# Optimization experiments

Hardware: AMD Instinct MI355X
Metric: run time of the kernel (lower is better)

## Reference

```python
import jax, jax.numpy as jnp
import numpy as np

HEADS = 8
EPS = 1e-5


def setup_inputs() -> dict:
    key = jax.random.key(0)
    B, N, C = 32, 4096, 256
    headc = C // HEADS
    x = jax.random.normal(key, (B, N, C), dtype=jnp.float32)
    return {
        "x": x,
        "kln_weight": jnp.ones((HEADS, 1, headc), dtype=jnp.float32),
        "kln_bias": jnp.zeros((HEADS, 1, headc), dtype=jnp.float32),
        "vln_weight": jnp.ones((HEADS, 1, headc), dtype=jnp.float32),
        "vln_bias": jnp.zeros((HEADS, 1, headc), dtype=jnp.float32),
    }


def _ln(t, w, b, headc):
    # Faithful to the torch module: unbiased std (ddof=1), eps added to std (not var).
    m = jnp.mean(t, axis=-1, keepdims=True)
    d = t - m
    std = jnp.sqrt(jnp.sum(d * d, axis=-1, keepdims=True) / (headc - 1))
    return w * (d / (std + EPS)) + b


def reference(x, kln_weight, kln_bias, vln_weight, vln_bias):
    B, N, C = x.shape
    headc = C // HEADS
    # [B, H, N, D]
    qkv = x.reshape(B, N, HEADS, headc).transpose(0, 2, 1, 3)
    k = _ln(qkv, kln_weight, kln_bias, headc)
    v = _ln(qkv, vln_weight, vln_bias, headc)
    # k^T v : [B, H, D, D], scaled by 1/N
    kv = jnp.einsum("bhnd,bhne->bhde", k, v) / N
    # q (k^T v): [B, H, N, D]
    out = jnp.einsum("bhnd,bhde->bhne", qkv, kv)
    out = out.transpose(0, 2, 1, 3).reshape(B, N, C)
    return out + x
```

## Files before the change

kernel.cpp:

```cpp
#include <hip/hip_runtime.h>

#define H_ 8
#define D_ 32
#define B_ 32
#define N_ 4096
#define C_ 256
#define EPS_ 1e-5f

#define SLOT_ 1088

typedef __attribute__((ext_vector_type(8))) short bf16x8;
typedef __attribute__((ext_vector_type(4))) float f32x4;

__device__ __forceinline__ short f2bf(float f) {
    unsigned u = __builtin_bit_cast(unsigned, f);
    unsigned r = (u + 0x7FFFu + ((u >> 16) & 1u)) >> 16;
    return (short)r;
}

__device__ __forceinline__ int uidx(int r, int c) {
    return r * 40 + ((r >> 3) & 3) * 16 + c;
}

__global__ __launch_bounds__(256, 4)
void k1_skv(const float* __restrict__ x, float* __restrict__ Pws)
{
    __shared__ short ubuf[256 * 40 + 64];

    const int tid  = threadIdx.x;
    const int bh   = blockIdx.x >> 2;
    const int q4   = blockIdx.x & 3;
    const int b    = bh >> 3;
    const int h    = bh & 7;
    const int lane = tid & 63;
    const int wave = tid >> 6;
    const int g    = lane >> 4;
    const int cL   = lane & 15;

    f32x4 acc[2][2] = {};
    f32x4 tq[2] = {};

    bf16x8 ones;
    #pragma unroll
    for (int j = 0; j < 8; ++j) ones[j] = (short)0x3F80;

    const float* xbase = x + ((size_t)b * N_ + q4 * 1024 + tid) * C_ + h * D_;

    float4 xA[8], xB[8];
    #pragma unroll
    for (int c = 0; c < 8; ++c)
        xA[c] = reinterpret_cast<const float4*>(xbase)[c];

    auto body = [&](const float4 (&xr)[8], float4 (&nx)[8], int it, bool pf) {
        if (pf) {
            const float* p = xbase + (size_t)(it + 1) * 256 * C_;
            #pragma unroll
            for (int c = 0; c < 8; ++c)
                nx[c] = reinterpret_cast<const float4*>(p)[c];
        }

        float sum = 0.f, sq = 0.f;
        #pragma unroll
        for (int c = 0; c < 8; ++c) {
            const float4 a = xr[c];
            sum += a.x + a.y + a.z + a.w;
            sq = fmaf(a.x, a.x, fmaf(a.y, a.y, fmaf(a.z, a.z, fmaf(a.w, a.w, sq))));
        }
        const float m   = sum * (1.f / 32.f);
        const float ss  = fmaxf(sq - sum * m, 0.f);
        const float inv = 1.f / (sqrtf(ss * (1.f / 31.f)) + EPS_);

        {
            const int base = tid * 40 + ((tid >> 3) & 3) * 16;
            #pragma unroll
            for (int q = 0; q < 4; ++q) {
                const float4 a0 = xr[q * 2 + 0];
                const float4 a1 = xr[q * 2 + 1];
                bf16x8 wv;
                wv[0] = f2bf((a0.x - m) * inv); wv[1] = f2bf((a0.y - m) * inv);
                wv[2] = f2bf((a0.z - m) * inv); wv[3] = f2bf((a0.w - m) * inv);
                wv[4] = f2bf((a1.x - m) * inv); wv[5] = f2bf((a1.y - m) * inv);
                wv[6] = f2bf((a1.z - m) * inv); wv[7] = f2bf((a1.w - m) * inv);
                *reinterpret_cast<bf16x8*>(&ubuf[base + q * 8]) = wv;
            }
        }
        asm volatile("s_waitcnt lgkmcnt(0)" ::: "memory");

        #pragma unroll
        for (int ks = 0; ks < 2; ++ks) {
            const int R0 = wave * 64 + ks * 32 + 8 * g;
            bf16x8 F0, F1;
            #pragma unroll
            for (int j = 0; j < 8; ++j) {
                const int base = uidx(R0 + j, cL);
                F0[j] = ubuf[base];
                F1[j] = ubuf[base + 16];
            }
            tq[0] = __builtin_amdgcn_mfma_f32_16x16x32_bf16(ones, F0, tq[0], 0, 0, 0);
            tq[1] = __builtin_amdgcn_mfma_f32_16x16x32_bf16(ones, F1, tq[1], 0, 0, 0);
            acc[0][0] = __builtin_amdgcn_mfma_f32_16x16x32_bf16(F0, F0, acc[0][0], 0, 0, 0);
            acc[0][1] = __builtin_amdgcn_mfma_f32_16x16x32_bf16(F0, F1, acc[0][1], 0, 0, 0);
            acc[1][0] = __builtin_amdgcn_mfma_f32_16x16x32_bf16(F1, F0, acc[1][0], 0, 0, 0);
            acc[1][1] = __builtin_amdgcn_mfma_f32_16x16x32_bf16(F1, F1, acc[1][1], 0, 0, 0);
        }
    };

    body(xA, xB, 0, true);
    body(xB, xA, 1, true);
    body(xA, xB, 2, true);
    body(xB, xA, 3, false);

    __syncthreads();
    float* sred = reinterpret_cast<float*>(ubuf);
    {
        float* dst = sred + wave * 1024;
        #pragma unroll
        for (int ca = 0; ca < 2; ++ca)
            #pragma unroll
            for (int cb = 0; cb < 2; ++cb)
                #pragma unroll
                for (int r = 0; r < 4; ++r)
                    dst[(ca * 16 + g * 4 + r) * D_ + cb * 16 + cL] = acc[ca][cb][r];
    }
    if (lane < 16) {
        sred[4096 + wave * 32 + cL]      = tq[0][0];
        sred[4096 + wave * 32 + 16 + cL] = tq[1][0];
    }
    __syncthreads();

    float* slot = Pws + (size_t)blockIdx.x * SLOT_;
    {
        const float4 c0 = *reinterpret_cast<const float4*>(&sred[tid * 4]);
        const float4 c1 = *reinterpret_cast<const float4*>(&sred[1024 + tid * 4]);
        const float4 c2 = *reinterpret_cast<const float4*>(&sred[2048 + tid * 4]);
        const float4 c3 = *reinterpret_cast<const float4*>(&sred[3072 + tid * 4]);
        float4 o;
        o.x = c0.x + c1.x + c2.x + c3.x;
        o.y = c0.y + c1.y + c2.y + c3.y;
        o.z = c0.z + c1.z + c2.z + c3.z;
        o.w = c0.w + c1.w + c2.w + c3.w;
        *reinterpret_cast<float4*>(slot + tid * 4) = o;
    }
    if (tid < D_)
        slot[1024 + tid] = sred[4096 + tid] + sred[4096 + 32 + tid]
                         + sred[4096 + 64 + tid] + sred[4096 + 96 + tid];
}

__global__ __launch_bounds__(256, 4)
void k2_out(const float* __restrict__ x, const float* __restrict__ Pws,
            const float* __restrict__ kw, const float* __restrict__ kb,
            const float* __restrict__ vw, const float* __restrict__ vb,
            float* __restrict__ out)
{
    __shared__ float xbuf[4 * C_];

    const int tid   = threadIdx.x;
    const int b     = blockIdx.x >> 6;
    const int chunk = blockIdx.x & 63;
    const int h     = tid >> 5;
    const int e     = tid & 31;
    const int bh    = b * 8 + h;

    const float* P0 = Pws + (size_t)(bh * 4 + 0) * SLOT_;
    const float* P1 = Pws + (size_t)(bh * 4 + 1) * SLOT_;
    const float* P2 = Pws + (size_t)(bh * 4 + 2) * SLOT_;
    const float* P3 = Pws + (size_t)(bh * 4 + 3) * SLOT_;

    const float wve  = vw[h * D_ + e];
    const float bve  = vb[h * D_ + e];
    const float Te   = P0[1024 + e] + P1[1024 + e] + P2[1024 + e] + P3[1024 + e];
    const float invN = 1.f / (float)N_;

    float kvc[32];
    #pragma unroll
    for (int d = 0; d < D_; ++d) {
        const float Sde = P0[d * D_ + e] + P1[d * D_ + e]
                        + P2[d * D_ + e] + P3[d * D_ + e];
        const float Td  = P0[1024 + d] + P1[1024 + d] + P2[1024 + d] + P3[1024 + d];
        const float wkd = kw[h * D_ + d];
        const float bkd = kb[h * D_ + d];
        kvc[d] = invN * (wkd * (wve * Sde + bve * Td) + bkd * wve * Te)
               + bkd * bve;
    }

    for (int it = 0; it < 16; ++it) {
        const int r0 = chunk * 64 + it * 4;
        const float* xrow = x + ((size_t)b * N_ + r0) * C_;
        const float4 xv = reinterpret_cast<const float4*>(xrow)[tid];
        __syncthreads();
        reinterpret_cast<float4*>(xbuf)[tid] = xv;
        __syncthreads();

        float res[4];
        #pragma unroll
        for (int r = 0; r < 4; ++r) {
            const float4* xr4 = reinterpret_cast<const float4*>(xbuf + r * C_ + h * D_);
            float dot = 0.f;
            #pragma unroll
            for (int c = 0; c < 8; ++c) {
                const float4 a = xr4[c];
                dot += a.x * kvc[c * 4 + 0] + a.y * kvc[c * 4 + 1]
                     + a.z * kvc[c * 4 + 2] + a.w * kvc[c * 4 + 3];
            }
            res[r] = dot + xbuf[r * C_ + tid];
        }
        float* orow = out + ((size_t)b * N_ + r0) * C_;
        #pragma unroll
        for (int r = 0; r < 4; ++r) orow[r * C_ + tid] = res[r];
    }
}

extern "C" void kernel_launch(void* const* d_in, const int* in_sizes, int n_in,
                              void* d_out, int out_size, void* d_ws, size_t ws_size,
                              hipStream_t stream)
{
    const float* x  = (const float*)d_in[0];
    const float* kw = (const float*)d_in[1];
    const float* kb = (const float*)d_in[2];
    const float* vw = (const float*)d_in[3];
    const float* vb = (const float*)d_in[4];
    float* outp = (float*)d_out;

    float* Pws = (float*)d_ws;

    k1_skv<<<dim3(B_ * H_ * 4), dim3(256), 0, stream>>>(x, Pws);
    k2_out<<<dim3(B_ * 64), dim3(256), 0, stream>>>(x, Pws, kw, kb, vw, vb, outp);
}
```

Before: 101.3 us.

## Split kv reduction into separate kernel and pipeline output pass per wave

Moves the per-(b,h) reduction of partial S/T sums and the LN-affine fold into a new small kernel that writes a finished 32x32 kv matrix, so the output kernel no longer redoes that reduction in every block. The output kernel now has each wave handle two heads of a 64-column slice, double-buffers x rows in per-wave LDS with register prefetch, and drops the block-wide __syncthreads. This adds a third kernel launch and an extra round trip through the kv buffer in exchange for less redundant work and fewer barriers in the bandwidth-bound output pass.

```diff
diff --git a/kernel.cpp b/kernel.cpp
--- a/kernel.cpp
+++ b/kernel.cpp
@@ -147,66 +147,104 @@
 }
 
 __global__ __launch_bounds__(256, 4)
-void k2_out(const float* __restrict__ x, const float* __restrict__ Pws,
-            const float* __restrict__ kw, const float* __restrict__ kb,
-            const float* __restrict__ vw, const float* __restrict__ vb,
-            float* __restrict__ out)
-{
-    __shared__ float xbuf[4 * C_];
-
-    const int tid   = threadIdx.x;
-    const int b     = blockIdx.x >> 6;
-    const int chunk = blockIdx.x & 63;
-    const int h     = tid >> 5;
-    const int e     = tid & 31;
-    const int bh    = b * 8 + h;
+void k_red(const float* __restrict__ Pws,
+           const float* __restrict__ kw, const float* __restrict__ kb,
+           const float* __restrict__ vw, const float* __restrict__ vb,
+           float* __restrict__ kvF)
+{
+    const int bh  = blockIdx.x;
+    const int h   = bh & 7;
+    const int tid = threadIdx.x;
+    const int d   = tid >> 3;
+    const int e0  = (tid & 7) * 4;
 
     const float* P0 = Pws + (size_t)(bh * 4 + 0) * SLOT_;
     const float* P1 = Pws + (size_t)(bh * 4 + 1) * SLOT_;
     const float* P2 = Pws + (size_t)(bh * 4 + 2) * SLOT_;
     const float* P3 = Pws + (size_t)(bh * 4 + 3) * SLOT_;
-
-    const float wve  = vw[h * D_ + e];
-    const float bve  = vb[h * D_ + e];
-    const float Te   = P0[1024 + e] + P1[1024 + e] + P2[1024 + e] + P3[1024 + e];
     const float invN = 1.f / (float)N_;
 
+    const float4 s0 = *reinterpret_cast<const float4*>(P0 + d * D_ + e0);
+    const float4 s1 = *reinterpret_cast<const float4*>(P1 + d * D_ + e0);
+    const float4 s2 = *reinterpret_cast<const float4*>(P2 + d * D_ + e0);
+    const float4 s3 = *reinterpret_cast<const float4*>(P3 + d * D_ + e0);
+    float Sde[4] = { s0.x + s1.x + s2.x + s3.x, s0.y + s1.y + s2.y + s3.y,
+                     s0.z + s1.z + s2.z + s3.z, s0.w + s1.w + s2.w + s3.w };
+
+    const float Td  = P0[1024 + d] + P1[1024 + d] + P2[1024 + d] + P3[1024 + d];
+    const float wkd = kw[h * D_ + d];
+    const float bkd = kb[h * D_ + d];
+
+    float4 o;
+    float* op = &o.x;
+    #pragma unroll
+    for (int j = 0; j < 4; ++j) {
+        const int e = e0 + j;
+        const float Te  = P0[1024 + e] + P1[1024 + e] + P2[1024 + e] + P3[1024 + e];
+        const float wve = vw[h * D_ + e];
+        const float bve = vb[h * D_ + e];
+        op[j] = invN * (wkd * (wve * Sde[j] + bve * Td) + bkd * wve * Te)
+              + bkd * bve;
+    }
+    *reinterpret_cast<float4*>(kvF + (size_t)bh * 1024 + tid * 4) = o;
+}
+
+__global__ __launch_bounds__(256, 4)
+void k2_out(const float* __restrict__ x, const float* __restrict__ kvF,
+            float* __restrict__ out)
+{
+    __shared__ float lds[4][2][256];
+
+    const int tid  = threadIdx.x;
+    const int lane = tid & 63;
+    const int w    = tid >> 6;
+    const int hloc = lane >> 5;
+    const int e    = lane & 31;
+    const int R0   = blockIdx.x * 64;
+    const int b    = R0 >> 12;
+    const int n0   = R0 & (N_ - 1);
+    const int h    = 2 * w + hloc;
+
+    const float* kvp = kvF + ((size_t)(b * H_ + h)) * 1024 + e;
     float kvc[32];
     #pragma unroll
-    for (int d = 0; d < D_; ++d) {
-        const float Sde = P0[d * D_ + e] + P1[d * D_ + e]
-                        + P2[d * D_ + e] + P3[d * D_ + e];
-        const float Td  = P0[1024 + d] + P1[1024 + d] + P2[1024 + d] + P3[1024 + d];
-        const float wkd = kw[h * D_ + d];
-        const float bkd = kb[h * D_ + d];
-        kvc[d] = invN * (wkd * (wve * Sde + bve * Td) + bkd * wve * Te)
-               + bkd * bve;
-    }
-
-    for (int it = 0; it < 16; ++it) {
-        const int r0 = chunk * 64 + it * 4;
-        const float* xrow = x + ((size_t)b * N_ + r0) * C_;
-        const float4 xv = reinterpret_cast<const float4*>(xrow)[tid];
-        __syncthreads();
-        reinterpret_cast<float4*>(xbuf)[tid] = xv;
-        __syncthreads();
-
-        float res[4];
+    for (int d = 0; d < D_; ++d) kvc[d] = kvp[d * D_];
+
+    const int lrow = lane >> 4;
+    const int lcol = (lane & 15) * 4;
+    const float* xg = x + ((size_t)b * N_ + n0 + lrow) * C_ + w * 64 + lcol;
+    float* og = out + ((size_t)b * N_ + n0) * C_ + w * 64 + hloc * 32 + e;
+
+    float* buf0 = &lds[w][0][0];
+    float* buf1 = &lds[w][1][0];
+    const int wslot = lrow * 64 + lcol;
+
+    float4 pA = *reinterpret_cast<const float4*>(xg);
+    float4 pB = *reinterpret_cast<const float4*>(xg + (size_t)4 * C_);
+
+    #pragma unroll 4
+    for (int t = 0; t < 16; ++t) {
+        float* buf = (t & 1) ? buf1 : buf0;
+        *reinterpret_cast<float4*>(buf + wslot) = pA;
+        pA = pB;
+        if (t + 2 < 16)
+            pB = *reinterpret_cast<const float4*>(xg + (size_t)(t + 2) * 4 * C_);
+        asm volatile("s_waitcnt lgkmcnt(0)" ::: "memory");
+
         #pragma unroll
         for (int r = 0; r < 4; ++r) {
-            const float4* xr4 = reinterpret_cast<const float4*>(xbuf + r * C_ + h * D_);
+            const float4* row4 =
+                reinterpret_cast<const float4*>(buf + r * 64 + hloc * 32);
             float dot = 0.f;
             #pragma unroll
             for (int c = 0; c < 8; ++c) {
-                const float4 a = xr4[c];
+                const float4 a = row4[c];
                 dot += a.x * kvc[c * 4 + 0] + a.y * kvc[c * 4 + 1]
                      + a.z * kvc[c * 4 + 2] + a.w * kvc[c * 4 + 3];
             }
-            res[r] = dot + xbuf[r * C_ + tid];
-        }
-        float* orow = out + ((size_t)b * N_ + r0) * C_;
-        #pragma unroll
-        for (int r = 0; r < 4; ++r) orow[r * C_ + tid] = res[r];
+            const float resx = buf[r * 64 + hloc * 32 + e];
+            og[(size_t)(t * 4 + r) * C_] = dot + resx;
+        }
     }
 }
 
@@ -222,7 +260,9 @@
     float* outp = (float*)d_out;
 
     float* Pws = (float*)d_ws;
+    float* kvF = Pws + (size_t)1024 * SLOT_;
 
     k1_skv<<<dim3(B_ * H_ * 4), dim3(256), 0, stream>>>(x, Pws);
-    k2_out<<<dim3(B_ * 64), dim3(256), 0, stream>>>(x, Pws, kw, kb, vw, vb, outp);
-}
+    k_red<<<dim3(B_ * H_), dim3(256), 0, stream>>>(Pws, kw, kb, vw, vb, kvF);
+    k2_out<<<dim3(B_ * N_ / 64), dim3(256), 0, stream>>>(x, kvF, outp);
+}
```

Result: faster. 83.40 us (-17.6%).

## Move kv partial reduction into a separate kernel and fold residual into kv

Applied to the files above, without the earlier changes.

Adds a small kernel that reduces the four per-block partial sums into a final 32x32 kv matrix per (batch, head) and folds the identity into its diagonal, so the residual add becomes part of the matmul. The output kernel then loads precomputed kv values instead of every block redundantly reducing partials and applying the LayerNorm affine terms. This removes 64x duplicated reduction work per batch, at the cost of an extra kernel launch and a workspace round-trip.

```diff
diff --git a/kernel.cpp b/kernel.cpp
--- a/kernel.cpp
+++ b/kernel.cpp
@@ -147,9 +147,52 @@
 }
 
 __global__ __launch_bounds__(256, 4)
-void k2_out(const float* __restrict__ x, const float* __restrict__ Pws,
-            const float* __restrict__ kw, const float* __restrict__ kb,
-            const float* __restrict__ vw, const float* __restrict__ vb,
+void k_red(const float* __restrict__ Pws,
+           const float* __restrict__ kw, const float* __restrict__ kb,
+           const float* __restrict__ vw, const float* __restrict__ vb,
+           float* __restrict__ kvF)
+{
+    const int bh  = blockIdx.x;
+    const int h   = bh & 7;
+    const int tid = threadIdx.x;
+    const int d   = tid >> 3;
+    const int e0  = (tid & 7) * 4;
+
+    const float* P0 = Pws + (size_t)(bh * 4 + 0) * SLOT_;
+    const float* P1 = Pws + (size_t)(bh * 4 + 1) * SLOT_;
+    const float* P2 = Pws + (size_t)(bh * 4 + 2) * SLOT_;
+    const float* P3 = Pws + (size_t)(bh * 4 + 3) * SLOT_;
+    const float invN = 1.f / (float)N_;
+
+    const float4 s0 = *reinterpret_cast<const float4*>(P0 + d * D_ + e0);
+    const float4 s1 = *reinterpret_cast<const float4*>(P1 + d * D_ + e0);
+    const float4 s2 = *reinterpret_cast<const float4*>(P2 + d * D_ + e0);
+    const float4 s3 = *reinterpret_cast<const float4*>(P3 + d * D_ + e0);
+    float Sde[4] = { s0.x + s1.x + s2.x + s3.x, s0.y + s1.y + s2.y + s3.y,
+                     s0.z + s1.z + s2.z + s3.z, s0.w + s1.w + s2.w + s3.w };
+
+    const float Td  = P0[1024 + d] + P1[1024 + d] + P2[1024 + d] + P3[1024 + d];
+    const float wkd = kw[h * D_ + d];
+    const float bkd = kb[h * D_ + d];
+
+    float4 o;
+    float* op = &o.x;
+    #pragma unroll
+    for (int j = 0; j < 4; ++j) {
+        const int e = e0 + j;
+        const float Te  = P0[1024 + e] + P1[1024 + e] + P2[1024 + e] + P3[1024 + e];
+        const float wve = vw[h * D_ + e];
+        const float bve = vb[h * D_ + e];
+        float v = invN * (wkd * (wve * Sde[j] + bve * Td) + bkd * wve * Te)
+                + bkd * bve;
+        if (d == e) v += 1.0f;
+        op[j] = v;
+    }
+    *reinterpret_cast<float4*>(kvF + (size_t)bh * 1024 + d * D_ + e0) = o;
+}
+
+__global__ __launch_bounds__(256, 4)
+void k2_out(const float* __restrict__ x, const float* __restrict__ kvF,
             float* __restrict__ out)
 {
     __shared__ float xbuf[4 * C_];
@@ -161,27 +204,10 @@
     const int e     = tid & 31;
     const int bh    = b * 8 + h;
 
-    const float* P0 = Pws + (size_t)(bh * 4 + 0) * SLOT_;
-    const float* P1 = Pws + (size_t)(bh * 4 + 1) * SLOT_;
-    const float* P2 = Pws + (size_t)(bh * 4 + 2) * SLOT_;
-    const float* P3 = Pws + (size_t)(bh * 4 + 3) * SLOT_;
-
-    const float wve  = vw[h * D_ + e];
-    const float bve  = vb[h * D_ + e];
-    const float Te   = P0[1024 + e] + P1[1024 + e] + P2[1024 + e] + P3[1024 + e];
-    const float invN = 1.f / (float)N_;
-
+    const float* kvp = kvF + (size_t)bh * 1024 + e;
     float kvc[32];
     #pragma unroll
-    for (int d = 0; d < D_; ++d) {
-        const float Sde = P0[d * D_ + e] + P1[d * D_ + e]
-                        + P2[d * D_ + e] + P3[d * D_ + e];
-        const float Td  = P0[1024 + d] + P1[1024 + d] + P2[1024 + d] + P3[1024 + d];
-        const float wkd = kw[h * D_ + d];
-        const float bkd = kb[h * D_ + d];
-        kvc[d] = invN * (wkd * (wve * Sde + bve * Td) + bkd * wve * Te)
-               + bkd * bve;
-    }
+    for (int d = 0; d < D_; ++d) kvc[d] = kvp[d * D_];
 
     for (int it = 0; it < 16; ++it) {
         const int r0 = chunk * 64 + it * 4;
@@ -202,7 +228,7 @@
                 dot += a.x * kvc[c * 4 + 0] + a.y * kvc[c * 4 + 1]
                      + a.z * kvc[c * 4 + 2] + a.w * kvc[c * 4 + 3];
             }
-            res[r] = dot + xbuf[r * C_ + tid];
+            res[r] = dot;
         }
         float* orow = out + ((size_t)b * N_ + r0) * C_;
         #pragma unroll
@@ -222,7 +248,9 @@
     float* outp = (float*)d_out;
 
     float* Pws = (float*)d_ws;
+    float* kvF = Pws + (size_t)1024 * SLOT_;
 
     k1_skv<<<dim3(B_ * H_ * 4), dim3(256), 0, stream>>>(x, Pws);
-    k2_out<<<dim3(B_ * 64), dim3(256), 0, stream>>>(x, Pws, kw, kb, vw, vb, outp);
-}
+    k_red<<<dim3(B_ * H_), dim3(256), 0, stream>>>(Pws, kw, kb, vw, vb, kvF);
+    k2_out<<<dim3(B_ * 64), dim3(256), 0, stream>>>(x, kvF, outp);
+}
```

Result: faster. 84.82 us (-16.2%).
